# Performance work log

Hardware: AMD Instinct MI355X
Metric: run time of the kernel (lower is better)

Reference implementation:

```python
import jax, jax.numpy as jnp
import numpy as np

D_MODEL = 1024
NUM_HEADS = 16
HEAD_DIM = D_MODEL // NUM_HEADS


def setup_inputs() -> dict:
    key = jax.random.key(0)
    ks = jax.random.split(key, 9)
    s = 1.0 / np.sqrt(D_MODEL)
    x = jax.random.normal(ks[0], (4, 2048, D_MODEL), dtype=jnp.float32)
    Wq = jax.random.uniform(ks[1], (D_MODEL, D_MODEL), jnp.float32, -s, s)
    bq = jax.random.uniform(ks[2], (D_MODEL,), jnp.float32, -s, s)
    Wk = jax.random.uniform(ks[3], (D_MODEL, D_MODEL), jnp.float32, -s, s)
    bk = jax.random.uniform(ks[4], (D_MODEL,), jnp.float32, -s, s)
    Wv = jax.random.uniform(ks[5], (D_MODEL, D_MODEL), jnp.float32, -s, s)
    bv = jax.random.uniform(ks[6], (D_MODEL,), jnp.float32, -s, s)
    Wo = jax.random.uniform(ks[7], (D_MODEL, D_MODEL), jnp.float32, -s, s)
    bo = jax.random.uniform(ks[8], (D_MODEL,), jnp.float32, -s, s)
    return {"x": x, "Wq": Wq, "bq": bq, "Wk": Wk, "bk": bk,
            "Wv": Wv, "bv": bv, "Wo": Wo, "bo": bo}


def reference(x, Wq, bq, Wk, bk, Wv, bv, Wo, bo):
    B, S, D = x.shape
    H, hd = NUM_HEADS, HEAD_DIM
    # QKV projections (torch Linear: x @ W^T + b)
    q = (x @ Wq.T + bq).reshape(B, S, H, hd).transpose(0, 2, 1, 3)  # [B,H,S,hd]
    k = (x @ Wk.T + bk).reshape(B, S, H, hd).transpose(0, 2, 1, 3)
    v = (x @ Wv.T + bv).reshape(B, S, H, hd).transpose(0, 2, 1, 3)
    scores = jnp.einsum('bhqd,bhkd->bhqk', q, k) / jnp.sqrt(jnp.float32(hd))
    attn = jax.nn.softmax(scores, axis=-1)  # dropout is identity in eval
    ctx = jnp.einsum('bhqk,bhkd->bhqd', attn, v)
    ctx = ctx.transpose(0, 2, 1, 3).reshape(B, S, D)
    return ctx @ Wo.T + bo
```

## Files before the change

kernel.cpp:

```cpp
#include <hip/hip_runtime.h>

typedef __bf16 bf16;
typedef __bf16 bf16x4 __attribute__((ext_vector_type(4)));
typedef __bf16 bf16x8 __attribute__((ext_vector_type(8)));
typedef float  f32x4  __attribute__((ext_vector_type(4)));
typedef float  f32x16 __attribute__((ext_vector_type(16)));
typedef unsigned int u32x4v __attribute__((ext_vector_type(4)));

#define NB   4
#define SEQ  2048
#define DM   1024
#define NH   16
#define HD   64
#define BHN  (NB*NH)
#define MTOT (NB*SEQ)
#define ELEMS ((size_t)MTOT*DM)
#define WELEMS (DM*DM)
#define QSCALE 0.18033688011112042f

__device__ __forceinline__ void gload16(void* lds, const void* g) {
  __builtin_amdgcn_global_load_lds(
      (const __attribute__((address_space(1))) void*)g,
      (__attribute__((address_space(3))) void*)lds, 16, 0, 0);
}

__device__ __forceinline__ f32x4 mfma16(bf16x8 a, bf16x8 b, f32x4 c) {
  return __builtin_amdgcn_mfma_f32_16x16x32_bf16(a, b, c, 0, 0, 0);
}
__device__ __forceinline__ f32x16 mfma32(bf16x8 a, bf16x8 b, f32x16 c) {
  return __builtin_amdgcn_mfma_f32_32x32x16_bf16(a, b, c, 0, 0, 0);
}
__device__ __forceinline__ unsigned cvtpk(float lo, float hi) {
  unsigned r;
  asm("v_cvt_pk_bf16_f32 %0, %1, %2" : "=v"(r) : "v"(lo), "v"(hi));
  return r;
}
__device__ __forceinline__ float exp2a(float x) {
  float r;
  asm("v_exp_f32 %0, %1" : "=v"(r) : "v"(x));
  return r;
}

__global__ __launch_bounds__(256) void cvt_all(
    const float* __restrict__ x, bf16* __restrict__ xb,
    const float* __restrict__ w0, const float* __restrict__ w1,
    const float* __restrict__ w2, const float* __restrict__ w3,
    bf16* __restrict__ wb)
{
  int y = blockIdx.y;
  const float* src; bf16* dst; int nblk;
  if (y < 4) {
    src = (y == 0) ? w0 : (y == 1) ? w1 : (y == 2) ? w2 : w3;
    dst = wb + (size_t)y * WELEMS;
    nblk = WELEMS / 1024;
  } else {
    src = x; dst = xb; nblk = (int)(ELEMS / 1024);
  }
  if (blockIdx.x >= nblk) return;
  int i = blockIdx.x * 1024 + threadIdx.x * 4;
  f32x4 v = *(const f32x4*)(src + i);
  bf16x4 o;
#pragma unroll
  for (int j = 0; j < 4; j++) o[j] = (bf16)v[j];
  *(bf16x4*)(dst + i) = o;
}

#define GEMM_CORE(A_, W_)                                                      \
  __shared__ __align__(16) bf16 lds_a[128*32];                                 \
  __shared__ __align__(16) bf16 lds_b[128*32];                                 \
  const int K = 1024;                                                          \
  int tid = threadIdx.x, wid = tid >> 6, lane = tid & 63;                      \
  int m0 = blockIdx.y * 128, n0 = blockIdx.x * 128;                            \
  int wr = wid >> 1, wc = wid & 1;                                             \
  int c15 = lane & 15, hi = lane >> 4;                                         \
  int srow = lane >> 2, scol = (lane & 3) * 8;                                 \
  const bf16* gA = (A_) + (m0 + wid*32 + srow) * K + scol;                     \
  const bf16* gB = (W_) + (n0 + wid*32 + srow) * K + scol;                     \
  bf16* la = lds_a + wid*1024;                                                 \
  bf16* lb = lds_b + wid*1024;                                                 \
  f32x4 acc[4][4] = {};                                                        \
  for (int k0 = 0; k0 < K; k0 += 32) {                                         \
    __syncthreads();                                                           \
    gload16(la,       gA + k0);                                                \
    gload16(la + 512, gA + 16*K + k0);                                         \
    gload16(lb,       gB + k0);                                                \
    gload16(lb + 512, gB + 16*K + k0);                                         \
    __syncthreads();                                                           \
    bf16x8 af[4], bfr[4];                                                      \
    _Pragma("unroll")                                                          \
    for (int i = 0; i < 4; i++)                                                \
      af[i]  = *(const bf16x8*)(lds_a + (wr*64 + i*16 + c15)*32 + hi*8);       \
    _Pragma("unroll")                                                          \
    for (int i = 0; i < 4; i++)                                                \
      bfr[i] = *(const bf16x8*)(lds_b + (wc*64 + i*16 + c15)*32 + hi*8);       \
    _Pragma("unroll")                                                          \
    for (int mi = 0; mi < 4; mi++)                                             \
      _Pragma("unroll")                                                        \
      for (int ni = 0; ni < 4; ni++)                                           \
        acc[mi][ni] = mfma16(af[mi], bfr[ni], acc[mi][ni]);                    \
  }

__global__ __launch_bounds__(256) void gemm_out(
    const bf16* __restrict__ A, const bf16* __restrict__ W,
    const float* __restrict__ bias, float* __restrict__ C)
{
  GEMM_CORE(A, W)
#pragma unroll
  for (int mi = 0; mi < 4; mi++) {
#pragma unroll
    for (int ni = 0; ni < 4; ni++) {
      int col = n0 + wc*64 + ni*16 + c15;
      float bvv = bias[col];
      int row = m0 + wr*64 + mi*16 + hi*4;
#pragma unroll
      for (int r = 0; r < 4; r++)
        C[(row + r)*DM + col] = acc[mi][ni][r] + bvv;
    }
  }
}

__global__ __launch_bounds__(512, 2) void gemm_qkv256(
    const bf16* __restrict__ A, const bf16* __restrict__ Wb3,
    const float* __restrict__ bq, const float* __restrict__ bk,
    const float* __restrict__ bv,
    bf16* __restrict__ Qb, bf16* __restrict__ Kb, bf16* __restrict__ Vtb)
{
  __shared__ __align__(16) bf16 la[2][256*64];
  __shared__ __align__(16) bf16 lb[2][128*64];

  const int K = 1024;
  int tid = threadIdx.x, wid = tid >> 6, lane = tid & 63;
  int wr = wid >> 1, wc = wid & 1;
  int c15 = lane & 15, hi = lane >> 4, l7 = lane & 7;

  int orig = blockIdx.x;
  int xcd = orig & 7, j = orig >> 3;
  int by = xcd * 4 + (j & 3);
  int bx = j >> 2;
  int m0 = by * 256, n0 = bx * 128;
  int z  = n0 >> 10;
  const float* bias = (z == 0) ? bq : (z == 1) ? bk : bv;

  int r8 = lane >> 3;
  int cu = (lane & 7) ^ r8;

  const bf16* gA = A   + (size_t)m0 * K;
  const bf16* gW = Wb3 + (size_t)n0 * K;

#define STA(buf, h, kt)                                                        \
  {                                                                            \
    _Pragma("unroll")                                                          \
    for (int op = 0; op < 2; op++) {                                           \
      int rowl = (h)*128 + wid*16 + op*8 + r8;                                 \
      gload16(&la[buf][((h)*128 + wid*16 + op*8)*64],                          \
              gA + (size_t)rowl*K + (kt)*64 + cu*8);                           \
    }                                                                          \
  }
#define STB(buf, kt)                                                           \
  {                                                                            \
    _Pragma("unroll")                                                          \
    for (int op = 0; op < 2; op++) {                                           \
      int rowl = wid*16 + op*8 + r8;                                           \
      gload16(&lb[buf][(wid*16 + op*8)*64],                                    \
              gW + (size_t)rowl*K + (kt)*64 + cu*8);                           \
    }                                                                          \
  }

  f32x4 acc[4][4] = {};
  const int NT = K / 64;

  STB(0, 0);
  STA(0, 0, 0);
  STA(0, 1, 0);

  for (int t = 0; t < NT; ++t) {
    int cb = t & 1, nb = cb ^ 1;
    asm volatile("s_waitcnt vmcnt(2)" ::: "memory");
    __builtin_amdgcn_s_barrier();
    asm volatile("" ::: "memory");

    bf16x8 af0[2][2], af1[2][2], bf0[2][2], bf1[2][2];

#pragma unroll
    for (int mi = 0; mi < 2; mi++)
#pragma unroll
      for (int kk = 0; kk < 2; kk++)
        af0[mi][kk] = *(const bf16x8*)(&la[cb][(wr*32 + mi*16 + c15)*64 + (((kk*4 + hi) ^ l7) * 8)]);
#pragma unroll
    for (int ni = 0; ni < 2; ni++)
#pragma unroll
      for (int kk = 0; kk < 2; kk++)
        bf0[ni][kk] = *(const bf16x8*)(&lb[cb][(wc*64 + ni*16 + c15)*64 + (((kk*4 + hi) ^ l7) * 8)]);
    if (t + 1 < NT) STB(nb, t + 1);
    __builtin_amdgcn_s_setprio(1);
#pragma unroll
    for (int mi = 0; mi < 2; mi++)
#pragma unroll
      for (int ni = 0; ni < 2; ni++)
#pragma unroll
        for (int kk = 0; kk < 2; kk++)
          acc[mi][ni] = mfma16(af0[mi][kk], bf0[ni][kk], acc[mi][ni]);
    __builtin_amdgcn_s_setprio(0);

#pragma unroll
    for (int ni = 0; ni < 2; ni++)
#pragma unroll
      for (int kk = 0; kk < 2; kk++)
        bf1[ni][kk] = *(const bf16x8*)(&lb[cb][(wc*64 + 32 + ni*16 + c15)*64 + (((kk*4 + hi) ^ l7) * 8)]);
    if (t + 1 < NT) STA(nb, 0, t + 1);
    __builtin_amdgcn_s_setprio(1);
#pragma unroll
    for (int mi = 0; mi < 2; mi++)
#pragma unroll
      for (int ni = 0; ni < 2; ni++)
#pragma unroll
        for (int kk = 0; kk < 2; kk++)
          acc[mi][2 + ni] = mfma16(af0[mi][kk], bf1[ni][kk], acc[mi][2 + ni]);
    __builtin_amdgcn_s_setprio(0);

    if (t + 1 < NT) { asm volatile("s_waitcnt vmcnt(4)" ::: "memory"); }
    else            { asm volatile("s_waitcnt vmcnt(0)" ::: "memory"); }
    __builtin_amdgcn_s_barrier();
    asm volatile("" ::: "memory");

#pragma unroll
    for (int mi = 0; mi < 2; mi++)
#pragma unroll
      for (int kk = 0; kk < 2; kk++)
        af1[mi][kk] = *(const bf16x8*)(&la[cb][(128 + wr*32 + mi*16 + c15)*64 + (((kk*4 + hi) ^ l7) * 8)]);
    if (t + 1 < NT) STA(nb, 1, t + 1);
    __builtin_amdgcn_s_setprio(1);
#pragma unroll
    for (int mi = 0; mi < 2; mi++)
#pragma unroll
      for (int ni = 0; ni < 2; ni++)
#pragma unroll
        for (int kk = 0; kk < 2; kk++)
          acc[2 + mi][2 + ni] = mfma16(af1[mi][kk], bf1[ni][kk], acc[2 + mi][2 + ni]);
    __builtin_amdgcn_s_setprio(0);

    __builtin_amdgcn_s_setprio(1);
#pragma unroll
    for (int mi = 0; mi < 2; mi++)
#pragma unroll
      for (int ni = 0; ni < 2; ni++)
#pragma unroll
        for (int kk = 0; kk < 2; kk++)
          acc[2 + mi][ni] = mfma16(af1[mi][kk], bf0[ni][kk], acc[2 + mi][ni]);
    __builtin_amdgcn_s_setprio(0);
  }
#undef STA
#undef STB

#pragma unroll
  for (int mi = 0; mi < 4; mi++) {
    int rbase = m0 + ((mi < 2) ? (wr*32 + mi*16) : (128 + wr*32 + (mi - 2)*16)) + hi*4;
#pragma unroll
    for (int ni = 0; ni < 4; ni++) {
      int n  = n0 + wc*64 + ni*16 + c15;
      int cz = n & 1023;
      float bvv = bias[cz];
      int h = cz >> 6, d = cz & 63;
      int b = rbase >> 11, s = rbase & 2047;
      if (z < 2) {
        bf16* C = z ? Kb : Qb;
        float sc = z ? 1.0f : QSCALE;
#pragma unroll
        for (int r = 0; r < 4; r++)
          C[((b*NH + h)*SEQ + (s + r))*HD + d] = (bf16)((acc[mi][ni][r] + bvv) * sc);
      } else {
        bf16x4 o;
#pragma unroll
        for (int r = 0; r < 4; r++) o[r] = (bf16)(acc[mi][ni][r] + bvv);
        *(bf16x4*)(Vtb + ((size_t)(b*NH + h)*HD + d)*SEQ + s) = o;
      }
    }
  }
}

__global__ __launch_bounds__(256, 2) void attn(
    const bf16* __restrict__ Q, const bf16* __restrict__ Kin,
    const bf16* __restrict__ Vt, bf16* __restrict__ ctx)
{
  __shared__ __align__(16) bf16 kt[2][128*64];
  __shared__ __align__(16) bf16 vt[2][64*128];

  int tid = threadIdx.x, wid = tid >> 6, lane = tid & 63;
  int l31 = lane & 31, hi = lane >> 5, l7 = lane & 7;

  int orig = blockIdx.y * gridDim.x + blockIdx.x;
  int swz  = (orig & 7) * 64 + (orig >> 3);
  int bh   = swz >> 3, q0 = (swz & 7) * 256;

  const bf16* Qp = Q   + (size_t)bh*SEQ*HD;
  const bf16* Kp = Kin + (size_t)bh*SEQ*HD;
  const bf16* Vp = Vt  + (size_t)bh*HD*SEQ;
  int qw = q0 + wid*64;

  bf16x8 qf[2][4];
#pragma unroll
  for (int qt = 0; qt < 2; qt++)
#pragma unroll
    for (int dblk = 0; dblk < 4; dblk++)
      qf[qt][dblk] = *(const bf16x8*)(Qp + (size_t)(qw + qt*32 + l31)*HD + dblk*16 + hi*8);

  f32x16 po[2][2]  = {};
  f32x16 posum[2]  = {};

  bf16x8 onesv;
#pragma unroll
  for (int j = 0; j < 8; j++) onesv[j] = (bf16)1.0f;

  int r8 = lane >> 3;
  int ck = (lane & 7) ^ r8;
  int r16 = lane >> 4, c16v = lane & 15;

#define STAGE(buf, kv0)                                                        \
  {                                                                            \
    _Pragma("unroll")                                                          \
    for (int op = 0; op < 4; op++) {                                           \
      int rk = wid*32 + op*8 + r8;                                             \
      gload16(&kt[buf][(wid*32 + op*8)*64],                                    \
              Kp + (size_t)((kv0) + rk)*HD + ck*8);                            \
      int rv = wid*16 + op*4 + r16;                                            \
      gload16(&vt[buf][(wid*16 + op*4)*128],                                   \
              Vp + (size_t)rv*SEQ + (kv0) + ((c16v ^ (rv & 7))*8));            \
    }                                                                          \
  }

  STAGE(0, 0);
  __syncthreads();

  for (int it = 0; it < SEQ/128; ++it) {
    int cur = it & 1;
    if (it < SEQ/128 - 1) STAGE(cur ^ 1, (it + 1) * 128);

#pragma unroll
    for (int sub = 0; sub < 2; sub++) {
      f32x16 st[2][2] = {};
      __builtin_amdgcn_s_setprio(1);
#pragma unroll
      for (int kvt = 0; kvt < 2; kvt++) {
        int rowb = (sub*64 + kvt*32 + l31) * 64;
#pragma unroll
        for (int dblk = 0; dblk < 4; dblk++) {
          bf16x8 kf = *(const bf16x8*)(&kt[cur][rowb + (((dblk*2 + hi) ^ l7) * 8)]);
          st[0][kvt] = mfma32(kf, qf[0][dblk], st[0][kvt]);
          st[1][kvt] = mfma32(kf, qf[1][dblk], st[1][kvt]);
        }
      }
      __builtin_amdgcn_s_setprio(0);

      bf16x8 pa[2][2][2];
#pragma unroll
      for (int qt = 0; qt < 2; qt++) {
#pragma unroll
        for (int kvt = 0; kvt < 2; kvt++)
#pragma unroll
          for (int i = 0; i < 16; i++)
            st[qt][kvt][i] = exp2a(st[qt][kvt][i]);
#pragma unroll
        for (int kvt = 0; kvt < 2; kvt++)
#pragma unroll
          for (int cp = 0; cp < 2; cp++) {
            int m0 = 2*cp, m1 = 2*cp + 1;
            unsigned w0a = cvtpk(st[qt][kvt][4*m0+0], st[qt][kvt][4*m0+1]);
            unsigned w1a = cvtpk(st[qt][kvt][4*m0+2], st[qt][kvt][4*m0+3]);
            unsigned w0b = cvtpk(st[qt][kvt][4*m1+0], st[qt][kvt][4*m1+1]);
            unsigned w1b = cvtpk(st[qt][kvt][4*m1+2], st[qt][kvt][4*m1+3]);
            asm("v_permlane32_swap_b32 %0, %1" : "+v"(w0a), "+v"(w0b));
            asm("v_permlane32_swap_b32 %0, %1" : "+v"(w1a), "+v"(w1b));
            pa[qt][kvt][cp] = __builtin_bit_cast(bf16x8, (u32x4v){w0a, w1a, w0b, w1b});
          }
      }

      __builtin_amdgcn_s_setprio(1);
#pragma unroll
      for (int dt = 0; dt < 2; dt++) {
        int rowb = (dt*32 + l31) * 128;
#pragma unroll
        for (int c = 0; c < 4; c++) {
          bf16x8 vf = *(const bf16x8*)(&vt[cur][rowb + ((sub*8 + ((c*2 + hi) ^ l7)) * 8)]);
          po[0][dt] = mfma32(pa[0][c >> 1][c & 1], vf, po[0][dt]);
          po[1][dt] = mfma32(pa[1][c >> 1][c & 1], vf, po[1][dt]);
        }
      }
#pragma unroll
      for (int c = 0; c < 4; c++) {
        posum[0] = mfma32(pa[0][c >> 1][c & 1], onesv, posum[0]);
        posum[1] = mfma32(pa[1][c >> 1][c & 1], onesv, posum[1]);
      }
      __builtin_amdgcn_s_setprio(0);
    }

    __syncthreads();
  }
#undef STAGE

  int b = bh >> 4, h = bh & 15;
#pragma unroll
  for (int qt = 0; qt < 2; qt++)
#pragma unroll
    for (int reg = 0; reg < 16; reg++) {
      int qq = (reg & 3) + 8*(reg >> 2) + 4*hi;
      float inv = 1.0f / posum[qt][reg];
      int s = qw + qt*32 + qq;
      bf16* dst = ctx + (size_t)(b*SEQ + s)*DM + h*HD + l31;
      dst[0]  = (bf16)(po[qt][0][reg] * inv);
      dst[32] = (bf16)(po[qt][1][reg] * inv);
    }
}

extern "C" void kernel_launch(void* const* d_in, const int* in_sizes, int n_in,
                              void* d_out, int out_size, void* d_ws, size_t ws_size,
                              hipStream_t stream)
{
  const float* x  = (const float*)d_in[0];
  const float* Wq = (const float*)d_in[1];
  const float* bq = (const float*)d_in[2];
  const float* Wk = (const float*)d_in[3];
  const float* bk = (const float*)d_in[4];
  const float* Wv = (const float*)d_in[5];
  const float* bv = (const float*)d_in[6];
  const float* Wo = (const float*)d_in[7];
  const float* bo = (const float*)d_in[8];

  bf16* ws  = (bf16*)d_ws;
  bf16* xb  = ws;
  bf16* Wb  = ws + ELEMS;
  bf16* Qb  = ws + ELEMS + 4*WELEMS;
  bf16* Kb  = Qb + ELEMS;
  bf16* Vtb = Kb + ELEMS;
  bf16* ctx = xb;

  cvt_all<<<dim3(ELEMS/1024, 5), dim3(256), 0, stream>>>(x, xb, Wq, Wk, Wv, Wo, Wb);
  gemm_qkv256<<<dim3(768), dim3(512), 0, stream>>>(
      xb, Wb, bq, bk, bv, Qb, Kb, Vtb);
  attn<<<dim3(SEQ/256, BHN), dim3(256), 0, stream>>>(Qb, Kb, Vtb, ctx);
  gemm_out<<<dim3(DM/128, MTOT/128), dim3(256), 0, stream>>>(
      ctx, Wb + 3*WELEMS, bo, (float*)d_out);
}
```

Baseline: 184.0 us.

## Replace output GEMM with pipelined 256x128 kernel and shrink attention blocks

The simple 128x128 output projection GEMM is replaced by a 512-thread 256x128 tile kernel. It double-buffers LDS, issues staged async loads interleaved with MFMA phases, uses swizzled LDS and XCD-aware block remapping. The attention kernel moves from 4-wave blocks over 256 queries with 128-wide KV tiles to 2-wave blocks over 128 queries with 64-wide KV tiles. That halves LDS per block and allows more resident blocks. The aim is better latency hiding and occupancy, at the cost of more loop iterations and more blocks re-reading K/V.

```diff
diff --git a/kernel.cpp b/kernel.cpp
--- a/kernel.cpp
+++ b/kernel.cpp
@@ -65,59 +65,6 @@
   *(bf16x4*)(dst + i) = o;
 }
 
-#define GEMM_CORE(A_, W_)                                                      \
-  __shared__ __align__(16) bf16 lds_a[128*32];                                 \
-  __shared__ __align__(16) bf16 lds_b[128*32];                                 \
-  const int K = 1024;                                                          \
-  int tid = threadIdx.x, wid = tid >> 6, lane = tid & 63;                      \
-  int m0 = blockIdx.y * 128, n0 = blockIdx.x * 128;                            \
-  int wr = wid >> 1, wc = wid & 1;                                             \
-  int c15 = lane & 15, hi = lane >> 4;                                         \
-  int srow = lane >> 2, scol = (lane & 3) * 8;                                 \
-  const bf16* gA = (A_) + (m0 + wid*32 + srow) * K + scol;                     \
-  const bf16* gB = (W_) + (n0 + wid*32 + srow) * K + scol;                     \
-  bf16* la = lds_a + wid*1024;                                                 \
-  bf16* lb = lds_b + wid*1024;                                                 \
-  f32x4 acc[4][4] = {};                                                        \
-  for (int k0 = 0; k0 < K; k0 += 32) {                                         \
-    __syncthreads();                                                           \
-    gload16(la,       gA + k0);                                                \
-    gload16(la + 512, gA + 16*K + k0);                                         \
-    gload16(lb,       gB + k0);                                                \
-    gload16(lb + 512, gB + 16*K + k0);                                         \
-    __syncthreads();                                                           \
-    bf16x8 af[4], bfr[4];                                                      \
-    _Pragma("unroll")                                                          \
-    for (int i = 0; i < 4; i++)                                                \
-      af[i]  = *(const bf16x8*)(lds_a + (wr*64 + i*16 + c15)*32 + hi*8);       \
-    _Pragma("unroll")                                                          \
-    for (int i = 0; i < 4; i++)                                                \
-      bfr[i] = *(const bf16x8*)(lds_b + (wc*64 + i*16 + c15)*32 + hi*8);       \
-    _Pragma("unroll")                                                          \
-    for (int mi = 0; mi < 4; mi++)                                             \
-      _Pragma("unroll")                                                        \
-      for (int ni = 0; ni < 4; ni++)                                           \
-        acc[mi][ni] = mfma16(af[mi], bfr[ni], acc[mi][ni]);                    \
-  }
-
-__global__ __launch_bounds__(256) void gemm_out(
-    const bf16* __restrict__ A, const bf16* __restrict__ W,
-    const float* __restrict__ bias, float* __restrict__ C)
-{
-  GEMM_CORE(A, W)
-#pragma unroll
-  for (int mi = 0; mi < 4; mi++) {
-#pragma unroll
-    for (int ni = 0; ni < 4; ni++) {
-      int col = n0 + wc*64 + ni*16 + c15;
-      float bvv = bias[col];
-      int row = m0 + wr*64 + mi*16 + hi*4;
-#pragma unroll
-      for (int r = 0; r < 4; r++)
-        C[(row + r)*DM + col] = acc[mi][ni][r] + bvv;
-    }
-  }
-}
 
 __global__ __launch_bounds__(512, 2) void gemm_qkv256(
     const bf16* __restrict__ A, const bf16* __restrict__ Wb3,
@@ -278,19 +225,162 @@
   }
 }
 
-__global__ __launch_bounds__(256, 2) void attn(
+__global__ __launch_bounds__(512, 2) void gemm_out256(
+    const bf16* __restrict__ A, const bf16* __restrict__ W,
+    const float* __restrict__ bias, float* __restrict__ C)
+{
+  __shared__ __align__(16) bf16 la[2][256*64];
+  __shared__ __align__(16) bf16 lb[2][128*64];
+
+  const int K = 1024;
+  int tid = threadIdx.x, wid = tid >> 6, lane = tid & 63;
+  int wr = wid >> 1, wc = wid & 1;
+  int c15 = lane & 15, hi = lane >> 4, l7 = lane & 7;
+
+  int orig = blockIdx.x;
+  int xcd = orig & 7, j = orig >> 3;
+  int by = xcd * 4 + (j & 3);
+  int bx = j >> 2;
+  int m0 = by * 256, n0 = bx * 128;
+
+  int r8 = lane >> 3;
+  int cu = (lane & 7) ^ r8;
+
+  const bf16* gA = A + (size_t)m0 * K;
+  const bf16* gW = W + (size_t)n0 * K;
+
+#define STA(buf, h, kt)                                                        \
+  {                                                                            \
+    _Pragma("unroll")                                                          \
+    for (int op = 0; op < 2; op++) {                                           \
+      int rowl = (h)*128 + wid*16 + op*8 + r8;                                 \
+      gload16(&la[buf][((h)*128 + wid*16 + op*8)*64],                          \
+              gA + (size_t)rowl*K + (kt)*64 + cu*8);                           \
+    }                                                                          \
+  }
+#define STB(buf, kt)                                                           \
+  {                                                                            \
+    _Pragma("unroll")                                                          \
+    for (int op = 0; op < 2; op++) {                                           \
+      int rowl = wid*16 + op*8 + r8;                                           \
+      gload16(&lb[buf][(wid*16 + op*8)*64],                                    \
+              gW + (size_t)rowl*K + (kt)*64 + cu*8);                           \
+    }                                                                          \
+  }
+
+  f32x4 acc[4][4] = {};
+  const int NT = K / 64;
+
+  STB(0, 0);
+  STA(0, 0, 0);
+  STA(0, 1, 0);
+
+  for (int t = 0; t < NT; ++t) {
+    int cb = t & 1, nb = cb ^ 1;
+    asm volatile("s_waitcnt vmcnt(2)" ::: "memory");
+    __builtin_amdgcn_s_barrier();
+    asm volatile("" ::: "memory");
+
+    bf16x8 af0[2][2], af1[2][2], bf0[2][2], bf1[2][2];
+
+#pragma unroll
+    for (int mi = 0; mi < 2; mi++)
+#pragma unroll
+      for (int kk = 0; kk < 2; kk++)
+        af0[mi][kk] = *(const bf16x8*)(&la[cb][(wr*32 + mi*16 + c15)*64 + (((kk*4 + hi) ^ l7) * 8)]);
+#pragma unroll
+    for (int ni = 0; ni < 2; ni++)
+#pragma unroll
+      for (int kk = 0; kk < 2; kk++)
+        bf0[ni][kk] = *(const bf16x8*)(&lb[cb][(wc*64 + ni*16 + c15)*64 + (((kk*4 + hi) ^ l7) * 8)]);
+    if (t + 1 < NT) STB(nb, t + 1);
+    __builtin_amdgcn_s_setprio(1);
+#pragma unroll
+    for (int mi = 0; mi < 2; mi++)
+#pragma unroll
+      for (int ni = 0; ni < 2; ni++)
+#pragma unroll
+        for (int kk = 0; kk < 2; kk++)
+          acc[mi][ni] = mfma16(af0[mi][kk], bf0[ni][kk], acc[mi][ni]);
+    __builtin_amdgcn_s_setprio(0);
+
+#pragma unroll
+    for (int ni = 0; ni < 2; ni++)
+#pragma unroll
+      for (int kk = 0; kk < 2; kk++)
+        bf1[ni][kk] = *(const bf16x8*)(&lb[cb][(wc*64 + 32 + ni*16 + c15)*64 + (((kk*4 + hi) ^ l7) * 8)]);
+    if (t + 1 < NT) STA(nb, 0, t + 1);
+    __builtin_amdgcn_s_setprio(1);
+#pragma unroll
+    for (int mi = 0; mi < 2; mi++)
+#pragma unroll
+      for (int ni = 0; ni < 2; ni++)
+#pragma unroll
+        for (int kk = 0; kk < 2; kk++)
+          acc[mi][2 + ni] = mfma16(af0[mi][kk], bf1[ni][kk], acc[mi][2 + ni]);
+    __builtin_amdgcn_s_setprio(0);
+
+    if (t + 1 < NT) { asm volatile("s_waitcnt vmcnt(4)" ::: "memory"); }
+    else            { asm volatile("s_waitcnt vmcnt(0)" ::: "memory"); }
+    __builtin_amdgcn_s_barrier();
+    asm volatile("" ::: "memory");
+
+#pragma unroll
+    for (int mi = 0; mi < 2; mi++)
+#pragma unroll
+      for (int kk = 0; kk < 2; kk++)
+        af1[mi][kk] = *(const bf16x8*)(&la[cb][(128 + wr*32 + mi*16 + c15)*64 + (((kk*4 + hi) ^ l7) * 8)]);
+    if (t + 1 < NT) STA(nb, 1, t + 1);
+    __builtin_amdgcn_s_setprio(1);
+#pragma unroll
+    for (int mi = 0; mi < 2; mi++)
+#pragma unroll
+      for (int ni = 0; ni < 2; ni++)
+#pragma unroll
+        for (int kk = 0; kk < 2; kk++)
+          acc[2 + mi][2 + ni] = mfma16(af1[mi][kk], bf1[ni][kk], acc[2 + mi][2 + ni]);
+    __builtin_amdgcn_s_setprio(0);
+
+    __builtin_amdgcn_s_setprio(1);
+#pragma unroll
+    for (int mi = 0; mi < 2; mi++)
+#pragma unroll
+      for (int ni = 0; ni < 2; ni++)
+#pragma unroll
+        for (int kk = 0; kk < 2; kk++)
+          acc[2 + mi][ni] = mfma16(af1[mi][kk], bf0[ni][kk], acc[2 + mi][ni]);
+    __builtin_amdgcn_s_setprio(0);
+  }
+#undef STA
+#undef STB
+
+#pragma unroll
+  for (int mi = 0; mi < 4; mi++) {
+    int rbase = m0 + ((mi < 2) ? (wr*32 + mi*16) : (128 + wr*32 + (mi - 2)*16)) + hi*4;
+#pragma unroll
+    for (int ni = 0; ni < 4; ni++) {
+      int col = n0 + wc*64 + ni*16 + c15;
+      float bvv = bias[col];
+#pragma unroll
+      for (int r = 0; r < 4; r++)
+        C[(size_t)(rbase + r)*DM + col] = acc[mi][ni][r] + bvv;
+    }
+  }
+}
+
+__global__ __launch_bounds__(128, 4) void attn(
     const bf16* __restrict__ Q, const bf16* __restrict__ Kin,
     const bf16* __restrict__ Vt, bf16* __restrict__ ctx)
 {
-  __shared__ __align__(16) bf16 kt[2][128*64];
-  __shared__ __align__(16) bf16 vt[2][64*128];
+  __shared__ __align__(16) bf16 kt[2][64*64];
+  __shared__ __align__(16) bf16 vt[2][64*64];
 
   int tid = threadIdx.x, wid = tid >> 6, lane = tid & 63;
   int l31 = lane & 31, hi = lane >> 5, l7 = lane & 7;
 
   int orig = blockIdx.y * gridDim.x + blockIdx.x;
-  int swz  = (orig & 7) * 64 + (orig >> 3);
-  int bh   = swz >> 3, q0 = (swz & 7) * 256;
+  int swz  = (orig & 7) * 128 + (orig >> 3);
+  int bh   = swz >> 4, q0 = (swz & 15) * 128;
 
   const bf16* Qp = Q   + (size_t)bh*SEQ*HD;
   const bf16* Kp = Kin + (size_t)bh*SEQ*HD;
@@ -312,86 +402,79 @@
   for (int j = 0; j < 8; j++) onesv[j] = (bf16)1.0f;
 
   int r8 = lane >> 3;
-  int ck = (lane & 7) ^ r8;
-  int r16 = lane >> 4, c16v = lane & 15;
+  int c16s = (lane & 7) ^ r8;
 
 #define STAGE(buf, kv0)                                                        \
   {                                                                            \
     _Pragma("unroll")                                                          \
     for (int op = 0; op < 4; op++) {                                           \
-      int rk = wid*32 + op*8 + r8;                                             \
-      gload16(&kt[buf][(wid*32 + op*8)*64],                                    \
-              Kp + (size_t)((kv0) + rk)*HD + ck*8);                            \
-      int rv = wid*16 + op*4 + r16;                                            \
-      gload16(&vt[buf][(wid*16 + op*4)*128],                                   \
-              Vp + (size_t)rv*SEQ + (kv0) + ((c16v ^ (rv & 7))*8));            \
+      int rowl = wid*32 + op*8 + r8;                                           \
+      gload16(&kt[buf][(wid*32 + op*8)*64], Kp + (size_t)((kv0) + rowl)*HD + c16s*8); \
+      gload16(&vt[buf][(wid*32 + op*8)*64], Vp + (size_t)rowl*SEQ + (kv0) + c16s*8);  \
     }                                                                          \
   }
 
   STAGE(0, 0);
   __syncthreads();
 
-  for (int it = 0; it < SEQ/128; ++it) {
+  for (int it = 0; it < SEQ/64; ++it) {
     int cur = it & 1;
-    if (it < SEQ/128 - 1) STAGE(cur ^ 1, (it + 1) * 128);
-
-#pragma unroll
-    for (int sub = 0; sub < 2; sub++) {
-      f32x16 st[2][2] = {};
-      __builtin_amdgcn_s_setprio(1);
-#pragma unroll
-      for (int kvt = 0; kvt < 2; kvt++) {
-        int rowb = (sub*64 + kvt*32 + l31) * 64;
-#pragma unroll
-        for (int dblk = 0; dblk < 4; dblk++) {
-          bf16x8 kf = *(const bf16x8*)(&kt[cur][rowb + (((dblk*2 + hi) ^ l7) * 8)]);
-          st[0][kvt] = mfma32(kf, qf[0][dblk], st[0][kvt]);
-          st[1][kvt] = mfma32(kf, qf[1][dblk], st[1][kvt]);
+    if (it < SEQ/64 - 1) STAGE(cur ^ 1, (it + 1) * 64);
+
+    f32x16 st[2][2] = {};
+    __builtin_amdgcn_s_setprio(1);
+#pragma unroll
+    for (int kvt = 0; kvt < 2; kvt++) {
+      int rowb = (kvt*32 + l31) * 64;
+#pragma unroll
+      for (int dblk = 0; dblk < 4; dblk++) {
+        bf16x8 kf = *(const bf16x8*)(&kt[cur][rowb + (((dblk*2 + hi) ^ l7) * 8)]);
+        st[0][kvt] = mfma32(kf, qf[0][dblk], st[0][kvt]);
+        st[1][kvt] = mfma32(kf, qf[1][dblk], st[1][kvt]);
+      }
+    }
+    __builtin_amdgcn_s_setprio(0);
+
+    bf16x8 pa[2][2][2];
+#pragma unroll
+    for (int qt = 0; qt < 2; qt++) {
+#pragma unroll
+      for (int kvt = 0; kvt < 2; kvt++)
+#pragma unroll
+        for (int i = 0; i < 16; i++)
+          st[qt][kvt][i] = exp2a(st[qt][kvt][i]);
+#pragma unroll
+      for (int kvt = 0; kvt < 2; kvt++)
+#pragma unroll
+        for (int cp = 0; cp < 2; cp++) {
+          int m0 = 2*cp, m1 = 2*cp + 1;
+          unsigned w0a = cvtpk(st[qt][kvt][4*m0+0], st[qt][kvt][4*m0+1]);
+          unsigned w1a = cvtpk(st[qt][kvt][4*m0+2], st[qt][kvt][4*m0+3]);
+          unsigned w0b = cvtpk(st[qt][kvt][4*m1+0], st[qt][kvt][4*m1+1]);
+          unsigned w1b = cvtpk(st[qt][kvt][4*m1+2], st[qt][kvt][4*m1+3]);
+          asm("v_permlane32_swap_b32 %0, %1" : "+v"(w0a), "+v"(w0b));
+          asm("v_permlane32_swap_b32 %0, %1" : "+v"(w1a), "+v"(w1b));
+          pa[qt][kvt][cp] = __builtin_bit_cast(bf16x8, (u32x4v){w0a, w1a, w0b, w1b});
         }
+    }
+
+    __builtin_amdgcn_s_setprio(1);
+#pragma unroll
+    for (int dt = 0; dt < 2; dt++) {
+      int rowb = (dt*32 + l31) * 64;
+#pragma unroll
+      for (int c = 0; c < 4; c++) {
+        bf16x8 vf = *(const bf16x8*)(&vt[cur][rowb + (((c*2 + hi) ^ l7) * 8)]);
+        po[0][dt] = mfma32(pa[0][c >> 1][c & 1], vf, po[0][dt]);
+        po[1][dt] = mfma32(pa[1][c >> 1][c & 1], vf, po[1][dt]);
       }
-      __builtin_amdgcn_s_setprio(0);
-
-      bf16x8 pa[2][2][2];
-#pragma unroll
-      for (int qt = 0; qt < 2; qt++) {
-#pragma unroll
-        for (int kvt = 0; kvt < 2; kvt++)
-#pragma unroll
-          for (int i = 0; i < 16; i++)
-            st[qt][kvt][i] = exp2a(st[qt][kvt][i]);
-#pragma unroll
-        for (int kvt = 0; kvt < 2; kvt++)
-#pragma unroll
-          for (int cp = 0; cp < 2; cp++) {
-            int m0 = 2*cp, m1 = 2*cp + 1;
-            unsigned w0a = cvtpk(st[qt][kvt][4*m0+0], st[qt][kvt][4*m0+1]);
-            unsigned w1a = cvtpk(st[qt][kvt][4*m0+2], st[qt][kvt][4*m0+3]);
-            unsigned w0b = cvtpk(st[qt][kvt][4*m1+0], st[qt][kvt][4*m1+1]);
-            unsigned w1b = cvtpk(st[qt][kvt][4*m1+2], st[qt][kvt][4*m1+3]);
-            asm("v_permlane32_swap_b32 %0, %1" : "+v"(w0a), "+v"(w0b));
-            asm("v_permlane32_swap_b32 %0, %1" : "+v"(w1a), "+v"(w1b));
-            pa[qt][kvt][cp] = __builtin_bit_cast(bf16x8, (u32x4v){w0a, w1a, w0b, w1b});
-          }
-      }
-
-      __builtin_amdgcn_s_setprio(1);
-#pragma unroll
-      for (int dt = 0; dt < 2; dt++) {
-        int rowb = (dt*32 + l31) * 128;
-#pragma unroll
-        for (int c = 0; c < 4; c++) {
-          bf16x8 vf = *(const bf16x8*)(&vt[cur][rowb + ((sub*8 + ((c*2 + hi) ^ l7)) * 8)]);
-          po[0][dt] = mfma32(pa[0][c >> 1][c & 1], vf, po[0][dt]);
-          po[1][dt] = mfma32(pa[1][c >> 1][c & 1], vf, po[1][dt]);
-        }
-      }
-#pragma unroll
-      for (int c = 0; c < 4; c++) {
-        posum[0] = mfma32(pa[0][c >> 1][c & 1], onesv, posum[0]);
-        posum[1] = mfma32(pa[1][c >> 1][c & 1], onesv, posum[1]);
-      }
-      __builtin_amdgcn_s_setprio(0);
-    }
+    }
+#pragma unroll
+    for (int c = 0; c < 4; c++) {
+      posum[0] = mfma32(pa[0][c >> 1][c & 1], onesv, posum[0]);
+      posum[1] = mfma32(pa[1][c >> 1][c & 1], onesv, posum[1]);
+    }
+    __builtin_amdgcn_s_setprio(0);
 
     __syncthreads();
   }
@@ -436,7 +519,7 @@
   cvt_all<<<dim3(ELEMS/1024, 5), dim3(256), 0, stream>>>(x, xb, Wq, Wk, Wv, Wo, Wb);
   gemm_qkv256<<<dim3(768), dim3(512), 0, stream>>>(
       xb, Wb, bq, bk, bv, Qb, Kb, Vtb);
-  attn<<<dim3(SEQ/256, BHN), dim3(256), 0, stream>>>(Qb, Kb, Vtb, ctx);
-  gemm_out<<<dim3(DM/128, MTOT/128), dim3(256), 0, stream>>>(
+  attn<<<dim3(SEQ/128, BHN), dim3(128), 0, stream>>>(Qb, Kb, Vtb, ctx);
+  gemm_out256<<<dim3(256), dim3(512), 0, stream>>>(
       ctx, Wb + 3*WELEMS, bo, (float*)d_out);
 }
```

Result: slower. 220.9 us (+20.1%).
